# Optimization experiments

Measured on AMD Instinct MI355X. Metric: run time of the kernel, lower is better.

The kernel has to match this reference:

```python
import jax, jax.numpy as jnp
import numpy as np

B, S, D = 8, 2048, 4096   # batch, seq_len, llm_dim
H = 8                     # num_map_heads
AD = 7                    # action_dim
TD = 32                   # time_dim
HID = 256                 # hidden_dim
NBLK = 3                  # num_blocks
DH = D // H


def _layernorm(x, g, b, eps=1e-5):
    m = jnp.mean(x, axis=-1, keepdims=True)
    v = jnp.var(x, axis=-1, keepdims=True)
    return (x - m) * jax.lax.rsqrt(v + eps) * g + b


def _forward(llm_output, time, noisy_actions, probe, wq, wk, wv, bq, bk, bv,
             wo, bo, ln_g, ln_b, mlp_w1, mlp_b1, mlp_w2, mlp_b2,
             four_w, cond_w1, cond_b1, cond_w2, cond_b2,
             rin_w, rin_b, blk_ln_g, blk_ln_b, blk_w1, blk_b1, blk_w2, blk_b2,
             out_w, out_b):
    b = llm_output.shape[0]
    # --- MAPHead: learned probe attends over LLM tokens (q_len = 1) ---
    q = (jnp.broadcast_to(probe, (b, 1, D)) @ wq + bq).reshape(b, 1, H, DH)
    k = (llm_output @ wk + bk).reshape(b, S, H, DH)
    v = (llm_output @ wv + bv).reshape(b, S, H, DH)
    scores = jnp.einsum('bqhd,bkhd->bhqk', q, k) / jnp.sqrt(jnp.asarray(DH, q.dtype))
    attn = jax.nn.softmax(scores, axis=-1)
    ctx = jnp.einsum('bhqk,bkhd->bqhd', attn, v).reshape(b, 1, D)
    attn_out = ctx @ wo + bo                      # (b, 1, D)
    y = _layernorm(attn_out, ln_g, ln_b)
    h = jax.nn.gelu(y @ mlp_w1 + mlp_b1, approximate=False) @ mlp_w2 + mlp_b2
    pooled = (attn_out + h)[:, 0, :]              # (b, D)
    # --- diffusion eps-prediction network (Octo-style ScoreActor) ---
    f = 2.0 * jnp.pi * (time @ four_w.T)          # (b, TD//2) learned Fourier features
    ff = jnp.concatenate([jnp.cos(f), jnp.sin(f)], axis=-1)  # (b, TD)
    cond = jax.nn.swish(ff @ cond_w1 + cond_b1) @ cond_w2 + cond_b2
    x = jnp.concatenate([cond, pooled, noisy_actions], axis=-1)
    x = x @ rin_w + rin_b                         # (b, HID)
    for i in range(NBLK):                         # small fixed structural loop
        r = x
        x = _layernorm(x, blk_ln_g[i], blk_ln_b[i])
        x = jax.nn.swish(x @ blk_w1[i] + blk_b1[i]) @ blk_w2[i] + blk_b2[i]
        x = r + x
    x = jax.nn.swish(x)
    return x @ out_w + out_b                      # (b, AD) predicted eps


def setup_inputs() -> dict:
    key = jax.random.key(0)
    ks = iter(jax.random.split(key, 40))
    def p(shape, s=0.02):
        return jax.random.normal(next(ks), shape, dtype=jnp.float32) * s
    return {
        'llm_output': jax.random.normal(next(ks), (B, S, D), dtype=jnp.float32),
        'time': jax.random.uniform(next(ks), (B, 1), dtype=jnp.float32) * 20.0,
        'noisy_actions': jax.random.normal(next(ks), (B, AD), dtype=jnp.float32),
        'probe': p((1, 1, D)),
        'wq': p((D, D)), 'wk': p((D, D)), 'wv': p((D, D)),
        'bq': jnp.zeros((D,)), 'bk': jnp.zeros((D,)), 'bv': jnp.zeros((D,)),
        'wo': p((D, D)), 'bo': jnp.zeros((D,)),
        'ln_g': jnp.ones((D,)), 'ln_b': jnp.zeros((D,)),
        'mlp_w1': p((D, 4 * D)), 'mlp_b1': jnp.zeros((4 * D,)),
        'mlp_w2': p((4 * D, D)), 'mlp_b2': jnp.zeros((D,)),
        'four_w': p((TD // 2, 1), 1.0),
        'cond_w1': p((TD, 2 * TD)), 'cond_b1': jnp.zeros((2 * TD,)),
        'cond_w2': p((2 * TD, TD)), 'cond_b2': jnp.zeros((TD,)),
        'rin_w': p((TD + D + AD, HID)), 'rin_b': jnp.zeros((HID,)),
        'blk_ln_g': jnp.ones((NBLK, HID)), 'blk_ln_b': jnp.zeros((NBLK, HID)),
        'blk_w1': p((NBLK, HID, 4 * HID)), 'blk_b1': jnp.zeros((NBLK, 4 * HID)),
        'blk_w2': p((NBLK, 4 * HID, HID)), 'blk_b2': jnp.zeros((NBLK, HID)),
        'out_w': p((HID, AD)), 'out_b': jnp.zeros((AD,)),
    }


def reference(llm_output, time, noisy_actions, probe, wq, wk, wv, bq, bk, bv,
              wo, bo, ln_g, ln_b, mlp_w1, mlp_b1, mlp_w2, mlp_b2,
              four_w, cond_w1, cond_b1, cond_w2, cond_b2,
              rin_w, rin_b, blk_ln_g, blk_ln_b, blk_w1, blk_b1, blk_w2, blk_b2,
              out_w, out_b):
    return _forward(llm_output, time, noisy_actions, probe, wq, wk, wv, bq, bk, bv,
                    wo, bo, ln_g, ln_b, mlp_w1, mlp_b1, mlp_w2, mlp_b2,
                    four_w, cond_w1, cond_b1, cond_w2, cond_b2,
                    rin_w, rin_b, blk_ln_g, blk_ln_b, blk_w1, blk_b1, blk_w2, blk_b2,
                    out_w, out_b)
```

## Files before the change

kernel.cpp:

```cpp
#include <hip/hip_runtime.h>
#include <hip/hip_bf16.h>
#include <math.h>


#define DEV __device__ __forceinline__

DEV float warp_sum64(float v) {
    for (int o = 32; o > 0; o >>= 1) v += __shfl_down(v, o, 64);
    return v;
}

DEV float block_sum256(float v, float* sc) {
    v = warp_sum64(v);
    __syncthreads();
    if ((threadIdx.x & 63) == 0) sc[threadIdx.x >> 6] = v;
    __syncthreads();
    return sc[0] + sc[1] + sc[2] + sc[3];
}

DEV float block_max256(float v, float* sc) {
    for (int o = 32; o > 0; o >>= 1) v = fmaxf(v, __shfl_down(v, o, 64));
    __syncthreads();
    if ((threadIdx.x & 63) == 0) sc[threadIdx.x >> 6] = v;
    __syncthreads();
    return fmaxf(fmaxf(sc[0], sc[1]), fmaxf(sc[2], sc[3]));
}

DEV float swish_f(float x) { return x / (1.f + expf(-x)); }
DEV float gelu_f(float x) { return 0.5f * x * (1.f + erff(x * 0.70710678118654752f)); }

template <int NB, int VEC>
__global__ __launch_bounds__(256) void gemv_part_kernel(
    const float* __restrict__ in, const float* __restrict__ W,
    float* __restrict__ part, int I, int J, int chunk) {
    extern __shared__ float lds[];
    int tid = threadIdx.x;
    int jb = blockIdx.x, ic = blockIdx.y;
    int i0 = ic * chunk;
    int cnt = min(chunk, I - i0);
    for (int idx = tid; idx < NB * cnt; idx += 256) {
        int b = idx / cnt, ii = idx - b * cnt;
        lds[b * chunk + ii] = in[(size_t)b * I + i0 + ii];
    }
    __syncthreads();
    int j = (jb * 256 + tid) * VEC;
    float acc[NB][VEC];
#pragma unroll
    for (int b = 0; b < NB; b++)
#pragma unroll
        for (int k = 0; k < VEC; k++) acc[b][k] = 0.f;
    int ii = 0;
    for (; ii + 4 <= cnt; ii += 4) {
        float w[4][VEC];
#pragma unroll
        for (int u = 0; u < 4; u++) {
            const float* wp = W + (size_t)(i0 + ii + u) * J + j;
            if constexpr (VEC == 4) {
                float4 t = *(const float4*)wp;
                w[u][0] = t.x; w[u][1] = t.y; w[u][2] = t.z; w[u][3] = t.w;
            } else {
                w[u][0] = wp[0];
            }
        }
#pragma unroll
        for (int u = 0; u < 4; u++)
#pragma unroll
            for (int b = 0; b < NB; b++) {
                float v = lds[b * chunk + ii + u];
#pragma unroll
                for (int k = 0; k < VEC; k++) acc[b][k] = fmaf(v, w[u][k], acc[b][k]);
            }
    }
    for (; ii < cnt; ii++) {
        const float* wp = W + (size_t)(i0 + ii) * J + j;
#pragma unroll
        for (int b = 0; b < NB; b++) {
            float v = lds[b * chunk + ii];
#pragma unroll
            for (int k = 0; k < VEC; k++) acc[b][k] = fmaf(v, wp[k], acc[b][k]);
        }
    }
#pragma unroll
    for (int b = 0; b < NB; b++) {
        float* pp = part + ((size_t)ic * NB + b) * J + j;
        if constexpr (VEC == 4) {
            float4 o; o.x = acc[b][0]; o.y = acc[b][1]; o.z = acc[b][2]; o.w = acc[b][3];
            *(float4*)pp = o;
        } else {
            pp[0] = acc[b][0];
        }
    }
}

__global__ __launch_bounds__(256) void reduce_kernel(
    const float* __restrict__ part, const float* __restrict__ bias,
    const float* __restrict__ res, float* __restrict__ out,
    int NBJ, int J, int nc, int act) {
    for (int idx = blockIdx.x * 256 + threadIdx.x; idx < NBJ; idx += gridDim.x * 256) {
        float s = 0.f;
        for (int c = 0; c < nc; c++) s += part[(size_t)c * NBJ + idx];
        int j = idx % J;
        if (bias) s += bias[j];
        if (res) s += res[idx];
        if (act == 1) s = gelu_f(s);
        else if (act == 2) s = swish_f(s);
        out[idx] = s;
    }
}

__global__ __launch_bounds__(256) void qw_kernel(
    const float* __restrict__ q, const float* __restrict__ wk,
    float* __restrict__ qw) {
    int gw = blockIdx.x * 4 + (threadIdx.x >> 6);
    int lane = threadIdx.x & 63;
    int h = gw >> 12, i = gw & 4095;
    const float* wrow = wk + (size_t)i * 4096 + h * 512;
    const float* qrow = q + h * 512;
    float acc = 0.f;
#pragma unroll
    for (int k = 0; k < 8; k++) acc = fmaf(qrow[lane + 64 * k], wrow[lane + 64 * k], acc);
    acc = warp_sum64(acc);
    if (lane == 0) qw[(size_t)h * 4096 + i] = acc;
}

__global__ __launch_bounds__(256) void scores_kernel(
    const float* __restrict__ llm, const float* __restrict__ qw,
    float* __restrict__ part) {
    __shared__ float qlds[8192];
    int tid = threadIdx.x;
    int rc = blockIdx.x, cc = blockIdx.y;
    for (int idx = tid; idx < 8192; idx += 256)
        qlds[idx] = qw[(size_t)(idx >> 10) * 4096 + cc * 1024 + (idx & 1023)];
    __syncthreads();
    int wid = tid >> 6, lane = tid & 63;
    int row0 = rc * 16 + wid * 4;
    const float* base = llm + (size_t)row0 * 4096 + cc * 1024 + lane * 4;
    float acc[4][8] = {};
    for (int it = 0; it < 4; ++it) {
        float4 lv[4];
#pragma unroll
        for (int r = 0; r < 4; r++) lv[r] = *(const float4*)(base + (size_t)r * 4096 + it * 256);
#pragma unroll
        for (int h = 0; h < 8; h++) {
            float4 q4 = *(const float4*)&qlds[h * 1024 + it * 256 + lane * 4];
#pragma unroll
            for (int r = 0; r < 4; r++)
                acc[r][h] += lv[r].x * q4.x + lv[r].y * q4.y + lv[r].z * q4.z + lv[r].w * q4.w;
        }
    }
#pragma unroll
    for (int r = 0; r < 4; r++)
#pragma unroll
        for (int h = 0; h < 8; h++) acc[r][h] = warp_sum64(acc[r][h]);
    if (lane == 0) {
#pragma unroll
        for (int r = 0; r < 4; r++) {
            int row = row0 + r;
            int b = row >> 11, s = row & 2047;
#pragma unroll
            for (int h = 0; h < 8; h++)
                part[((size_t)(cc * 8 + b) * 8 + h) * 2048 + s] = acc[r][h];
        }
    }
}

__global__ __launch_bounds__(256) void softmax_kernel(
    const float* __restrict__ part, float* __restrict__ attn) {
    __shared__ float sc[4];
    int bh = blockIdx.x, tid = threadIdx.x;
    float v[8];
    float mx = -1e30f;
#pragma unroll
    for (int k = 0; k < 8; k++) {
        int s = tid + k * 256;
        float x = 0.f;
        for (int cc = 0; cc < 4; cc++) x += part[((size_t)(cc * 64 + bh)) * 2048 + s];
        x *= 0.04419417382415922f;
        v[k] = x;
        mx = fmaxf(mx, x);
    }
    float M = block_max256(mx, sc);
    float sum = 0.f;
#pragma unroll
    for (int k = 0; k < 8; k++) { v[k] = expf(v[k] - M); sum += v[k]; }
    float Sv = block_sum256(sum, sc);
    float inv = 1.f / Sv;
#pragma unroll
    for (int k = 0; k < 8; k++) attn[(size_t)bh * 2048 + tid + k * 256] = v[k] * inv;
}

__global__ __launch_bounds__(256) void pooled_kernel(
    const float* __restrict__ llm, const float* __restrict__ attn,
    float* __restrict__ part) {
    __shared__ float alds[1024];
    int tid = threadIdx.x;
    int jb = blockIdx.x, sc = blockIdx.y, b = blockIdx.z;
    for (int idx = tid; idx < 1024; idx += 256) {
        int h = idx >> 7, sl = idx & 127;
        alds[idx] = attn[((size_t)(b * 8 + h)) * 2048 + sc * 128 + sl];
    }
    __syncthreads();
    int j = jb * 1024 + tid * 4;
    const float* lbase = llm + ((size_t)(b * 2048 + sc * 128)) * 4096 + j;
    float acc[8][4] = {};
    for (int si = 0; si < 128; si += 4) {
        float4 lv[4];
#pragma unroll
        for (int u = 0; u < 4; u++) lv[u] = *(const float4*)(lbase + (size_t)(si + u) * 4096);
#pragma unroll
        for (int u = 0; u < 4; u++)
#pragma unroll
            for (int h = 0; h < 8; h++) {
                float a = alds[h * 128 + si + u];
                acc[h][0] = fmaf(a, lv[u].x, acc[h][0]);
                acc[h][1] = fmaf(a, lv[u].y, acc[h][1]);
                acc[h][2] = fmaf(a, lv[u].z, acc[h][2]);
                acc[h][3] = fmaf(a, lv[u].w, acc[h][3]);
            }
    }
#pragma unroll
    for (int h = 0; h < 8; h++) {
        float4 o; o.x = acc[h][0]; o.y = acc[h][1]; o.z = acc[h][2]; o.w = acc[h][3];
        *(float4*)(part + ((size_t)(sc * 8 + b) * 8 + h) * 4096 + j) = o;
    }
}

__global__ __launch_bounds__(256) void ctx_gemv_kernel(
    const float* __restrict__ pooled, const float* __restrict__ wv,
    float* __restrict__ part) {
    __shared__ float plds[1024];
    int tid = threadIdx.x, jb = blockIdx.x, ic = blockIdx.y;
    int i0 = ic * 64, h0 = jb * 2;
    for (int idx = tid; idx < 1024; idx += 256) {
        int b = idx >> 7, r = idx & 127, hh = r >> 6, ii = r & 63;
        plds[(b * 2 + hh) * 64 + ii] = pooled[((size_t)(b * 8 + h0 + hh)) * 4096 + i0 + ii];
    }
    __syncthreads();
    int j = jb * 1024 + tid * 4;
    int hh = tid >> 7;
    float acc[8][4] = {};
    for (int ii = 0; ii < 64; ii += 4) {
        float4 w[4];
#pragma unroll
        for (int u = 0; u < 4; u++) w[u] = *(const float4*)(wv + (size_t)(i0 + ii + u) * 4096 + j);
#pragma unroll
        for (int u = 0; u < 4; u++)
#pragma unroll
            for (int b = 0; b < 8; b++) {
                float v = plds[(b * 2 + hh) * 64 + ii + u];
                acc[b][0] = fmaf(v, w[u].x, acc[b][0]);
                acc[b][1] = fmaf(v, w[u].y, acc[b][1]);
                acc[b][2] = fmaf(v, w[u].z, acc[b][2]);
                acc[b][3] = fmaf(v, w[u].w, acc[b][3]);
            }
    }
#pragma unroll
    for (int b = 0; b < 8; b++) {
        float4 o; o.x = acc[b][0]; o.y = acc[b][1]; o.z = acc[b][2]; o.w = acc[b][3];
        *(float4*)(part + ((size_t)ic * 8 + b) * 4096 + j) = o;
    }
}

__global__ __launch_bounds__(256) void ln_kernel(
    const float* __restrict__ x, const float* __restrict__ g,
    const float* __restrict__ be, float* __restrict__ out, int N) {
    __shared__ float sc[4];
    int b = blockIdx.x, tid = threadIdx.x;
    const float* xb = x + (size_t)b * N;
    float s = 0.f, s2 = 0.f;
    for (int i = tid; i < N; i += 256) { float v = xb[i]; s += v; s2 += v * v; }
    s = block_sum256(s, sc);
    s2 = block_sum256(s2, sc);
    float mean = s / N;
    float var = s2 / N - mean * mean;
    float rstd = rsqrtf(var + 1e-5f);
    float* ob = out + (size_t)b * N;
    for (int i = tid; i < N; i += 256) {
        float v = xb[i];
        ob[i] = (v - mean) * rstd * g[i] + be[i];
    }
}

__global__ __launch_bounds__(256) void cond_kernel(
    const float* __restrict__ time, const float* __restrict__ four_w,
    const float* __restrict__ w1, const float* __restrict__ b1,
    const float* __restrict__ w2, const float* __restrict__ b2,
    float* __restrict__ cond) {
    __shared__ float ffl[256];
    __shared__ float c1[512];
    int tid = threadIdx.x;
    {
        int b = tid >> 5, jj = tid & 31;
        float f = 6.283185307179586f * time[b] * four_w[jj & 15];
        ffl[tid] = (jj < 16) ? cosf(f) : sinf(f);
    }
    __syncthreads();
    for (int idx = tid; idx < 512; idx += 256) {
        int b = idx >> 6, jj = idx & 63;
        float s = b1[jj];
        for (int i = 0; i < 32; i++) s = fmaf(ffl[b * 32 + i], w1[i * 64 + jj], s);
        c1[idx] = swish_f(s);
    }
    __syncthreads();
    {
        int b = tid >> 5, jj = tid & 31;
        float s = b2[jj];
        for (int i = 0; i < 64; i++) s = fmaf(c1[b * 64 + i], w2[i * 32 + jj], s);
        cond[b * 32 + jj] = s;
    }
}

__global__ __launch_bounds__(256) void rin_gemv_kernel(
    const float* __restrict__ cond, const float* __restrict__ pfinal,
    const float* __restrict__ noisy, const float* __restrict__ W,
    float* __restrict__ part) {
    __shared__ float lds[512];
    int tid = threadIdx.x, ic = blockIdx.x;
    int i0 = ic * 64;
    int cnt = min(64, 4135 - i0);
    for (int idx = tid; idx < 8 * cnt; idx += 256) {
        int b = idx / cnt, ii = idx - b * cnt;
        int i = i0 + ii;
        float v;
        if (i < 32) v = cond[b * 32 + i];
        else if (i < 4128) v = pfinal[(size_t)b * 4096 + i - 32];
        else v = noisy[b * 7 + i - 4128];
        lds[b * 64 + ii] = v;
    }
    __syncthreads();
    int j = tid;
    float acc[8] = {};
#pragma unroll 4
    for (int ii = 0; ii < cnt; ii++) {
        float w = W[(size_t)(i0 + ii) * 256 + j];
#pragma unroll
        for (int b = 0; b < 8; b++) acc[b] = fmaf(lds[b * 64 + ii], w, acc[b]);
    }
#pragma unroll
    for (int b = 0; b < 8; b++) part[((size_t)ic * 8 + b) * 256 + j] = acc[b];
}

__global__ __launch_bounds__(256) void final_kernel(
    const float* __restrict__ x3, const float* __restrict__ out_w,
    const float* __restrict__ out_b, float* __restrict__ out) {
    __shared__ float sw[2048];
    int tid = threadIdx.x;
    for (int idx = tid; idx < 2048; idx += 256) sw[idx] = swish_f(x3[idx]);
    __syncthreads();
    if (tid < 56) {
        int b = tid / 7, a = tid - b * 7;
        float s = out_b[a];
        for (int i = 0; i < 256; i++) s = fmaf(sw[b * 256 + i], out_w[i * 7 + a], s);
        out[tid] = s;
    }
}

extern "C" void kernel_launch(void* const* d_in, const int* in_sizes, int n_in,
                              void* d_out, int out_size, void* d_ws, size_t ws_size,
                              hipStream_t stream) {
    const float* llm     = (const float*)d_in[0];
    const float* time_   = (const float*)d_in[1];
    const float* noisy   = (const float*)d_in[2];
    const float* probe   = (const float*)d_in[3];
    const float* wq      = (const float*)d_in[4];
    const float* wk      = (const float*)d_in[5];
    const float* wv      = (const float*)d_in[6];
    const float* bq      = (const float*)d_in[7];
    const float* bv      = (const float*)d_in[9];
    const float* wo      = (const float*)d_in[10];
    const float* bo      = (const float*)d_in[11];
    const float* ln_g    = (const float*)d_in[12];
    const float* ln_b    = (const float*)d_in[13];
    const float* mlp_w1  = (const float*)d_in[14];
    const float* mlp_b1  = (const float*)d_in[15];
    const float* mlp_w2  = (const float*)d_in[16];
    const float* mlp_b2  = (const float*)d_in[17];
    const float* four_w  = (const float*)d_in[18];
    const float* cond_w1 = (const float*)d_in[19];
    const float* cond_b1 = (const float*)d_in[20];
    const float* cond_w2 = (const float*)d_in[21];
    const float* cond_b2 = (const float*)d_in[22];
    const float* rin_w   = (const float*)d_in[23];
    const float* rin_b   = (const float*)d_in[24];
    const float* bln_g   = (const float*)d_in[25];
    const float* bln_b   = (const float*)d_in[26];
    const float* bw1     = (const float*)d_in[27];
    const float* bb1     = (const float*)d_in[28];
    const float* bw2     = (const float*)d_in[29];
    const float* bb2     = (const float*)d_in[30];
    const float* out_w   = (const float*)d_in[31];
    const float* out_b   = (const float*)d_in[32];

    float* ws = (float*)d_ws;
    const size_t A = (size_t)4 * 1024 * 1024;
    float* arena    = ws;
    float* q        = ws + A;
    float* qw       = q + 4096;
    float* attn     = qw + 32768;
    float* pooled   = attn + 131072;
    float* ctx      = pooled + 262144;
    float* attn_out = ctx + 32768;
    float* y        = attn_out + 32768;
    float* h1a      = y + 32768;
    float* pfinal   = h1a + 131072;
    float* cond     = pfinal + 32768;
    float* x0       = cond + 256;
    float* xln      = x0 + 2048;
    float* g1a      = xln + 2048;
    float* x1       = g1a + 8192;
    float* x2       = x1 + 2048;
    float* x3       = x2 + 2048;

    gemv_part_kernel<1, 4><<<dim3(4, 64), 256, 1 * 64 * 4, stream>>>(probe, wq, arena, 4096, 4096, 64);
    reduce_kernel<<<16, 256, 0, stream>>>(arena, bq, nullptr, q, 4096, 4096, 64, 0);
    qw_kernel<<<8192, 256, 0, stream>>>(q, wk, qw);
    scores_kernel<<<dim3(1024, 4), 256, 0, stream>>>(llm, qw, arena);
    softmax_kernel<<<64, 256, 0, stream>>>(arena, attn);
    pooled_kernel<<<dim3(4, 16, 8), 256, 0, stream>>>(llm, attn, arena);
    reduce_kernel<<<256, 256, 0, stream>>>(arena, nullptr, nullptr, pooled, 262144, 4096, 16, 0);
    ctx_gemv_kernel<<<dim3(4, 64), 256, 0, stream>>>(pooled, wv, arena);
    reduce_kernel<<<128, 256, 0, stream>>>(arena, bv, nullptr, ctx, 32768, 4096, 64, 0);
    gemv_part_kernel<8, 4><<<dim3(4, 64), 256, 8 * 64 * 4, stream>>>(ctx, wo, arena, 4096, 4096, 64);
    reduce_kernel<<<128, 256, 0, stream>>>(arena, bo, nullptr, attn_out, 32768, 4096, 64, 0);
    ln_kernel<<<8, 256, 0, stream>>>(attn_out, ln_g, ln_b, y, 4096);
    gemv_part_kernel<8, 4><<<dim3(16, 16), 256, 8 * 256 * 4, stream>>>(y, mlp_w1, arena, 4096, 16384, 256);
    reduce_kernel<<<256, 256, 0, stream>>>(arena, mlp_b1, nullptr, h1a, 131072, 16384, 16, 1);
    gemv_part_kernel<8, 4><<<dim3(4, 64), 256, 8 * 256 * 4, stream>>>(h1a, mlp_w2, arena, 16384, 4096, 256);
    reduce_kernel<<<128, 256, 0, stream>>>(arena, mlp_b2, attn_out, pfinal, 32768, 4096, 64, 0);

    cond_kernel<<<1, 256, 0, stream>>>(time_, four_w, cond_w1, cond_b1, cond_w2, cond_b2, cond);
    rin_gemv_kernel<<<65, 256, 0, stream>>>(cond, pfinal, noisy, rin_w, arena);
    reduce_kernel<<<8, 256, 0, stream>>>(arena, rin_b, nullptr, x0, 2048, 256, 65, 0);

    float* xs[4] = {x0, x1, x2, x3};
    for (int i = 0; i < 3; i++) {
        ln_kernel<<<8, 256, 0, stream>>>(xs[i], bln_g + i * 256, bln_b + i * 256, xln, 256);
        gemv_part_kernel<8, 1><<<dim3(4, 4), 256, 8 * 64 * 4, stream>>>(
            xln, bw1 + (size_t)i * 256 * 1024, arena, 256, 1024, 64);
        reduce_kernel<<<32, 256, 0, stream>>>(arena, bb1 + i * 1024, nullptr, g1a, 8192, 1024, 4, 2);
        gemv_part_kernel<8, 1><<<dim3(1, 16), 256, 8 * 64 * 4, stream>>>(
            g1a, bw2 + (size_t)i * 1024 * 256, arena, 1024, 256, 64);
        reduce_kernel<<<8, 256, 0, stream>>>(arena, bb2 + i * 256, xs[i], xs[i + 1], 2048, 256, 16, 0);
    }
    final_kernel<<<1, 256, 0, stream>>>(x3, out_w, out_b, (float*)d_out);
}
```

Before: 1.354 ms.

## Fuse pooled reduction into ctx GEMV, fuse residual blocks, retune GEMV splits

The pooled reduce kernel is removed, and ctx_k now sums the 16 sequence-chunk partials itself while filling shared memory. Each residual block's LayerNorm, first GEMV, swish and partial reduce become one kernel (rb1_k), and its second GEMV, bias and residual add become another (rb2_k). These cut launches and intermediate global round-trips. The generic GEMV now loads 8 float4 weight rows per iteration, drops its tail handling (chunk must divide evenly), and the MLP GEMVs use 128-row chunks with more partial blocks, giving more parallelism at the cost of larger reductions.

Result: faster. 1.302 ms (-3.8%).

```diff
diff --git a/kernel.cpp b/kernel.cpp
--- a/kernel.cpp
+++ b/kernel.cpp
@@ -29,70 +29,49 @@
 DEV float swish_f(float x) { return x / (1.f + expf(-x)); }
 DEV float gelu_f(float x) { return 0.5f * x * (1.f + erff(x * 0.70710678118654752f)); }
 
-template <int NB, int VEC>
-__global__ __launch_bounds__(256) void gemv_part_kernel(
+template <int NB>
+__global__ __launch_bounds__(256) void gemvp_k(
     const float* __restrict__ in, const float* __restrict__ W,
     float* __restrict__ part, int I, int J, int chunk) {
     extern __shared__ float lds[];
     int tid = threadIdx.x;
     int jb = blockIdx.x, ic = blockIdx.y;
     int i0 = ic * chunk;
-    int cnt = min(chunk, I - i0);
-    for (int idx = tid; idx < NB * cnt; idx += 256) {
-        int b = idx / cnt, ii = idx - b * cnt;
-        lds[b * chunk + ii] = in[(size_t)b * I + i0 + ii];
-    }
-    __syncthreads();
-    int j = (jb * 256 + tid) * VEC;
-    float acc[NB][VEC];
+    for (int idx = tid; idx < NB * chunk; idx += 256) {
+        int b = idx / chunk, ii = idx - b * chunk;
+        lds[idx] = in[(size_t)b * I + i0 + ii];
+    }
+    __syncthreads();
+    int j = (jb * 256 + tid) * 4;
+    float acc[NB][4];
 #pragma unroll
     for (int b = 0; b < NB; b++)
 #pragma unroll
-        for (int k = 0; k < VEC; k++) acc[b][k] = 0.f;
-    int ii = 0;
-    for (; ii + 4 <= cnt; ii += 4) {
-        float w[4][VEC];
-#pragma unroll
-        for (int u = 0; u < 4; u++) {
-            const float* wp = W + (size_t)(i0 + ii + u) * J + j;
-            if constexpr (VEC == 4) {
-                float4 t = *(const float4*)wp;
-                w[u][0] = t.x; w[u][1] = t.y; w[u][2] = t.z; w[u][3] = t.w;
-            } else {
-                w[u][0] = wp[0];
-            }
-        }
-#pragma unroll
-        for (int u = 0; u < 4; u++)
+        for (int k = 0; k < 4; k++) acc[b][k] = 0.f;
+    const float* wbase = W + (size_t)i0 * J + j;
+    for (int ii = 0; ii < chunk; ii += 8) {
+        float4 w[8];
+#pragma unroll
+        for (int u = 0; u < 8; u++) w[u] = *(const float4*)(wbase + (size_t)(ii + u) * J);
+#pragma unroll
+        for (int u = 0; u < 8; u++)
 #pragma unroll
             for (int b = 0; b < NB; b++) {
                 float v = lds[b * chunk + ii + u];
-#pragma unroll
-                for (int k = 0; k < VEC; k++) acc[b][k] = fmaf(v, w[u][k], acc[b][k]);
+                acc[b][0] = fmaf(v, w[u].x, acc[b][0]);
+                acc[b][1] = fmaf(v, w[u].y, acc[b][1]);
+                acc[b][2] = fmaf(v, w[u].z, acc[b][2]);
+                acc[b][3] = fmaf(v, w[u].w, acc[b][3]);
             }
     }
-    for (; ii < cnt; ii++) {
-        const float* wp = W + (size_t)(i0 + ii) * J + j;
-#pragma unroll
-        for (int b = 0; b < NB; b++) {
-            float v = lds[b * chunk + ii];
-#pragma unroll
-            for (int k = 0; k < VEC; k++) acc[b][k] = fmaf(v, wp[k], acc[b][k]);
-        }
-    }
 #pragma unroll
     for (int b = 0; b < NB; b++) {
-        float* pp = part + ((size_t)ic * NB + b) * J + j;
-        if constexpr (VEC == 4) {
-            float4 o; o.x = acc[b][0]; o.y = acc[b][1]; o.z = acc[b][2]; o.w = acc[b][3];
-            *(float4*)pp = o;
-        } else {
-            pp[0] = acc[b][0];
-        }
-    }
-}
-
-__global__ __launch_bounds__(256) void reduce_kernel(
+        float4 o; o.x = acc[b][0]; o.y = acc[b][1]; o.z = acc[b][2]; o.w = acc[b][3];
+        *(float4*)(part + ((size_t)ic * NB + b) * J + j) = o;
+    }
+}
+
+__global__ __launch_bounds__(256) void reduce_k(
     const float* __restrict__ part, const float* __restrict__ bias,
     const float* __restrict__ res, float* __restrict__ out,
     int NBJ, int J, int nc, int act) {
@@ -108,7 +87,7 @@
     }
 }
 
-__global__ __launch_bounds__(256) void qw_kernel(
+__global__ __launch_bounds__(256) void qw_k(
     const float* __restrict__ q, const float* __restrict__ wk,
     float* __restrict__ qw) {
     int gw = blockIdx.x * 4 + (threadIdx.x >> 6);
@@ -123,7 +102,7 @@
     if (lane == 0) qw[(size_t)h * 4096 + i] = acc;
 }
 
-__global__ __launch_bounds__(256) void scores_kernel(
+__global__ __launch_bounds__(256) void scores_k(
     const float* __restrict__ llm, const float* __restrict__ qw,
     float* __restrict__ part) {
     __shared__ float qlds[8192];
@@ -164,7 +143,7 @@
     }
 }
 
-__global__ __launch_bounds__(256) void softmax_kernel(
+__global__ __launch_bounds__(256) void softmax_k(
     const float* __restrict__ part, float* __restrict__ attn) {
     __shared__ float sc[4];
     int bh = blockIdx.x, tid = threadIdx.x;
@@ -189,7 +168,7 @@
     for (int k = 0; k < 8; k++) attn[(size_t)bh * 2048 + tid + k * 256] = v[k] * inv;
 }
 
-__global__ __launch_bounds__(256) void pooled_kernel(
+__global__ __launch_bounds__(256) void pooled_k(
     const float* __restrict__ llm, const float* __restrict__ attn,
     float* __restrict__ part) {
     __shared__ float alds[1024];
@@ -203,12 +182,12 @@
     int j = jb * 1024 + tid * 4;
     const float* lbase = llm + ((size_t)(b * 2048 + sc * 128)) * 4096 + j;
     float acc[8][4] = {};
-    for (int si = 0; si < 128; si += 4) {
-        float4 lv[4];
-#pragma unroll
-        for (int u = 0; u < 4; u++) lv[u] = *(const float4*)(lbase + (size_t)(si + u) * 4096);
-#pragma unroll
-        for (int u = 0; u < 4; u++)
+    for (int si = 0; si < 128; si += 8) {
+        float4 lv[8];
+#pragma unroll
+        for (int u = 0; u < 8; u++) lv[u] = *(const float4*)(lbase + (size_t)(si + u) * 4096);
+#pragma unroll
+        for (int u = 0; u < 8; u++)
 #pragma unroll
             for (int h = 0; h < 8; h++) {
                 float a = alds[h * 128 + si + u];
@@ -225,26 +204,30 @@
     }
 }
 
-__global__ __launch_bounds__(256) void ctx_gemv_kernel(
-    const float* __restrict__ pooled, const float* __restrict__ wv,
+__global__ __launch_bounds__(256) void ctx_k(
+    const float* __restrict__ ppart, const float* __restrict__ wv,
     float* __restrict__ part) {
     __shared__ float plds[1024];
     int tid = threadIdx.x, jb = blockIdx.x, ic = blockIdx.y;
     int i0 = ic * 64, h0 = jb * 2;
     for (int idx = tid; idx < 1024; idx += 256) {
         int b = idx >> 7, r = idx & 127, hh = r >> 6, ii = r & 63;
-        plds[(b * 2 + hh) * 64 + ii] = pooled[((size_t)(b * 8 + h0 + hh)) * 4096 + i0 + ii];
+        float s = 0.f;
+#pragma unroll 4
+        for (int sc = 0; sc < 16; sc++)
+            s += ppart[((size_t)(sc * 8 + b) * 8 + h0 + hh) * 4096 + i0 + ii];
+        plds[(b * 2 + hh) * 64 + ii] = s;
     }
     __syncthreads();
     int j = jb * 1024 + tid * 4;
     int hh = tid >> 7;
     float acc[8][4] = {};
-    for (int ii = 0; ii < 64; ii += 4) {
-        float4 w[4];
-#pragma unroll
-        for (int u = 0; u < 4; u++) w[u] = *(const float4*)(wv + (size_t)(i0 + ii + u) * 4096 + j);
-#pragma unroll
-        for (int u = 0; u < 4; u++)
+    for (int ii = 0; ii < 64; ii += 8) {
+        float4 w[8];
+#pragma unroll
+        for (int u = 0; u < 8; u++) w[u] = *(const float4*)(wv + (size_t)(i0 + ii + u) * 4096 + j);
+#pragma unroll
+        for (int u = 0; u < 8; u++)
 #pragma unroll
             for (int b = 0; b < 8; b++) {
                 float v = plds[(b * 2 + hh) * 64 + ii + u];
@@ -261,7 +244,7 @@
     }
 }
 
-__global__ __launch_bounds__(256) void ln_kernel(
+__global__ __launch_bounds__(256) void ln_k(
     const float* __restrict__ x, const float* __restrict__ g,
     const float* __restrict__ be, float* __restrict__ out, int N) {
     __shared__ float sc[4];
@@ -281,7 +264,7 @@
     }
 }
 
-__global__ __launch_bounds__(256) void cond_kernel(
+__global__ __launch_bounds__(256) void cond_k(
     const float* __restrict__ time, const float* __restrict__ four_w,
     const float* __restrict__ w1, const float* __restrict__ b1,
     const float* __restrict__ w2, const float* __restrict__ b2,
@@ -310,7 +293,7 @@
     }
 }
 
-__global__ __launch_bounds__(256) void rin_gemv_kernel(
+__global__ __launch_bounds__(256) void rin_k(
     const float* __restrict__ cond, const float* __restrict__ pfinal,
     const float* __restrict__ noisy, const float* __restrict__ W,
     float* __restrict__ part) {
@@ -340,7 +323,95 @@
     for (int b = 0; b < 8; b++) part[((size_t)ic * 8 + b) * 256 + j] = acc[b];
 }
 
-__global__ __launch_bounds__(256) void final_kernel(
+__global__ __launch_bounds__(256) void rb1_k(
+    const float* __restrict__ xin, const float* __restrict__ g,
+    const float* __restrict__ be, const float* __restrict__ W1,
+    const float* __restrict__ b1, float* __restrict__ g1) {
+    __shared__ float xn[2048];
+    __shared__ float red[2048];
+    __shared__ float sm[8], sv[8];
+    int tid = threadIdx.x, jb = blockIdx.x;
+    int b = tid >> 5, l = tid & 31;
+    float xv[8];
+    float s = 0.f, s2 = 0.f;
+#pragma unroll
+    for (int k = 0; k < 8; k++) {
+        float v = xin[tid * 8 + k];
+        xv[k] = v; s += v; s2 += v * v;
+    }
+    for (int o = 16; o > 0; o >>= 1) { s += __shfl_down(s, o, 32); s2 += __shfl_down(s2, o, 32); }
+    if (l == 0) { sm[b] = s; sv[b] = s2; }
+    __syncthreads();
+    float mean = sm[b] / 256.f;
+    float rstd = rsqrtf(sv[b] / 256.f - mean * mean + 1e-5f);
+#pragma unroll
+    for (int k = 0; k < 8; k++) {
+        int i = (tid * 8 + k) & 255;
+        xn[tid * 8 + k] = (xv[k] - mean) * rstd * g[i] + be[i];
+    }
+    __syncthreads();
+    int jj = tid & 63, ig = tid >> 6;
+    int j = jb * 64 + jj;
+    float acc[8] = {};
+    for (int i = ig * 64; i < ig * 64 + 64; i += 4) {
+        float w[4];
+#pragma unroll
+        for (int u = 0; u < 4; u++) w[u] = W1[(size_t)(i + u) * 1024 + j];
+#pragma unroll
+        for (int u = 0; u < 4; u++)
+#pragma unroll
+            for (int bb = 0; bb < 8; bb++) acc[bb] = fmaf(xn[bb * 256 + i + u], w[u], acc[bb]);
+    }
+#pragma unroll
+    for (int bb = 0; bb < 8; bb++) red[tid * 8 + bb] = acc[bb];
+    __syncthreads();
+#pragma unroll
+    for (int t = 0; t < 2; t++) {
+        int idx = tid * 2 + t;
+        int ojj = idx >> 3, ob = idx & 7;
+        float v = red[ojj * 8 + ob] + red[512 + ojj * 8 + ob] +
+                  red[1024 + ojj * 8 + ob] + red[1536 + ojj * 8 + ob];
+        v += b1[jb * 64 + ojj];
+        g1[(size_t)ob * 1024 + jb * 64 + ojj] = swish_f(v);
+    }
+}
+
+__global__ __launch_bounds__(256) void rb2_k(
+    const float* __restrict__ g1, const float* __restrict__ W2,
+    const float* __restrict__ b2, const float* __restrict__ xres,
+    float* __restrict__ xout) {
+    __shared__ float gl[8192];
+    __shared__ float red[2048];
+    int tid = threadIdx.x, jb = blockIdx.x;
+    for (int idx = tid * 4; idx < 8192; idx += 1024)
+        *(float4*)&gl[idx] = *(const float4*)&g1[idx];
+    __syncthreads();
+    int jj = tid & 15, ig = tid >> 4;
+    int j = jb * 16 + jj;
+    float acc[8] = {};
+    for (int i = ig * 64; i < ig * 64 + 64; i += 4) {
+        float w[4];
+#pragma unroll
+        for (int u = 0; u < 4; u++) w[u] = W2[(size_t)(i + u) * 256 + j];
+#pragma unroll
+        for (int u = 0; u < 4; u++)
+#pragma unroll
+            for (int bb = 0; bb < 8; bb++) acc[bb] = fmaf(gl[bb * 1024 + i + u], w[u], acc[bb]);
+    }
+#pragma unroll
+    for (int bb = 0; bb < 8; bb++) red[tid * 8 + bb] = acc[bb];
+    __syncthreads();
+    if (tid < 128) {
+        int ojj = tid >> 3, ob = tid & 7;
+        float v = 0.f;
+#pragma unroll
+        for (int ig2 = 0; ig2 < 16; ig2++) v += red[(ig2 * 16 + ojj) * 8 + ob];
+        int oj = jb * 16 + ojj;
+        xout[(size_t)ob * 256 + oj] = v + b2[oj] + xres[(size_t)ob * 256 + oj];
+    }
+}
+
+__global__ __launch_bounds__(256) void final_k(
     const float* __restrict__ x3, const float* __restrict__ out_w,
     const float* __restrict__ out_b, float* __restrict__ out) {
     __shared__ float sw[2048];
@@ -394,53 +465,48 @@
     float* ws = (float*)d_ws;
     const size_t A = (size_t)4 * 1024 * 1024;
     float* arena    = ws;
-    float* q        = ws + A;
+    float* arena2   = ws + A;
+    float* q        = arena2 + 2097152;
     float* qw       = q + 4096;
     float* attn     = qw + 32768;
-    float* pooled   = attn + 131072;
-    float* ctx      = pooled + 262144;
+    float* ctx      = attn + 131072;
     float* attn_out = ctx + 32768;
     float* y        = attn_out + 32768;
     float* h1a      = y + 32768;
     float* pfinal   = h1a + 131072;
     float* cond     = pfinal + 32768;
     float* x0       = cond + 256;
-    float* xln      = x0 + 2048;
-    float* g1a      = xln + 2048;
+    float* g1a      = x0 + 2048;
     float* x1       = g1a + 8192;
     float* x2       = x1 + 2048;
     float* x3       = x2 + 2048;
 
-    gemv_part_kernel<1, 4><<<dim3(4, 64), 256, 1 * 64 * 4, stream>>>(probe, wq, arena, 4096, 4096, 64);
-    reduce_kernel<<<16, 256, 0, stream>>>(arena, bq, nullptr, q, 4096, 4096, 64, 0);
-    qw_kernel<<<8192, 256, 0, stream>>>(q, wk, qw);
-    scores_kernel<<<dim3(1024, 4), 256, 0, stream>>>(llm, qw, arena);
-    softmax_kernel<<<64, 256, 0, stream>>>(arena, attn);
-    pooled_kernel<<<dim3(4, 16, 8), 256, 0, stream>>>(llm, attn, arena);
-    reduce_kernel<<<256, 256, 0, stream>>>(arena, nullptr, nullptr, pooled, 262144, 4096, 16, 0);
-    ctx_gemv_kernel<<<dim3(4, 64), 256, 0, stream>>>(pooled, wv, arena);
-    reduce_kernel<<<128, 256, 0, stream>>>(arena, bv, nullptr, ctx, 32768, 4096, 64, 0);
-    gemv_part_kernel<8, 4><<<dim3(4, 64), 256, 8 * 64 * 4, stream>>>(ctx, wo, arena, 4096, 4096, 64);
-    reduce_kernel<<<128, 256, 0, stream>>>(arena, bo, nullptr, attn_out, 32768, 4096, 64, 0);
-    ln_kernel<<<8, 256, 0, stream>>>(attn_out, ln_g, ln_b, y, 4096);
-    gemv_part_kernel<8, 4><<<dim3(16, 16), 256, 8 * 256 * 4, stream>>>(y, mlp_w1, arena, 4096, 16384, 256);
-    reduce_kernel<<<256, 256, 0, stream>>>(arena, mlp_b1, nullptr, h1a, 131072, 16384, 16, 1);
-    gemv_part_kernel<8, 4><<<dim3(4, 64), 256, 8 * 256 * 4, stream>>>(h1a, mlp_w2, arena, 16384, 4096, 256);
-    reduce_kernel<<<128, 256, 0, stream>>>(arena, mlp_b2, attn_out, pfinal, 32768, 4096, 64, 0);
-
-    cond_kernel<<<1, 256, 0, stream>>>(time_, four_w, cond_w1, cond_b1, cond_w2, cond_b2, cond);
-    rin_gemv_kernel<<<65, 256, 0, stream>>>(cond, pfinal, noisy, rin_w, arena);
-    reduce_kernel<<<8, 256, 0, stream>>>(arena, rin_b, nullptr, x0, 2048, 256, 65, 0);
+    gemvp_k<1><<<dim3(4, 64), 256, 64 * 4, stream>>>(probe, wq, arena, 4096, 4096, 64);
+    reduce_k<<<16, 256, 0, stream>>>(arena, bq, nullptr, q, 4096, 4096, 64, 0);
+    qw_k<<<8192, 256, 0, stream>>>(q, wk, qw);
+    scores_k<<<dim3(1024, 4), 256, 0, stream>>>(llm, qw, arena);
+    softmax_k<<<64, 256, 0, stream>>>(arena, attn);
+    pooled_k<<<dim3(4, 16, 8), 256, 0, stream>>>(llm, attn, arena);
+    ctx_k<<<dim3(4, 64), 256, 0, stream>>>(arena, wv, arena2);
+    reduce_k<<<32, 256, 0, stream>>>(arena2, bv, nullptr, ctx, 32768, 4096, 64, 0);
+    gemvp_k<8><<<dim3(4, 64), 256, 8 * 64 * 4, stream>>>(ctx, wo, arena, 4096, 4096, 64);
+    reduce_k<<<32, 256, 0, stream>>>(arena, bo, nullptr, attn_out, 32768, 4096, 64, 0);
+    ln_k<<<8, 256, 0, stream>>>(attn_out, ln_g, ln_b, y, 4096);
+    gemvp_k<8><<<dim3(16, 32), 256, 8 * 128 * 4, stream>>>(y, mlp_w1, arena, 4096, 16384, 128);
+    reduce_k<<<256, 256, 0, stream>>>(arena, mlp_b1, nullptr, h1a, 131072, 16384, 32, 1);
+    gemvp_k<8><<<dim3(4, 128), 256, 8 * 128 * 4, stream>>>(h1a, mlp_w2, arena, 16384, 4096, 128);
+    reduce_k<<<64, 256, 0, stream>>>(arena, mlp_b2, attn_out, pfinal, 32768, 4096, 128, 0);
+
+    cond_k<<<1, 256, 0, stream>>>(time_, four_w, cond_w1, cond_b1, cond_w2, cond_b2, cond);
+    rin_k<<<65, 256, 0, stream>>>(cond, pfinal, noisy, rin_w, arena);
+    reduce_k<<<8, 256, 0, stream>>>(arena, rin_b, nullptr, x0, 2048, 256, 65, 0);
 
     float* xs[4] = {x0, x1, x2, x3};
     for (int i = 0; i < 3; i++) {
-        ln_kernel<<<8, 256, 0, stream>>>(xs[i], bln_g + i * 256, bln_b + i * 256, xln, 256);
-        gemv_part_kernel<8, 1><<<dim3(4, 4), 256, 8 * 64 * 4, stream>>>(
-            xln, bw1 + (size_t)i * 256 * 1024, arena, 256, 1024, 64);
-        reduce_kernel<<<32, 256, 0, stream>>>(arena, bb1 + i * 1024, nullptr, g1a, 8192, 1024, 4, 2);
-        gemv_part_kernel<8, 1><<<dim3(1, 16), 256, 8 * 64 * 4, stream>>>(
-            g1a, bw2 + (size_t)i * 1024 * 256, arena, 1024, 256, 64);
-        reduce_kernel<<<8, 256, 0, stream>>>(arena, bb2 + i * 256, xs[i], xs[i + 1], 2048, 256, 16, 0);
-    }
-    final_kernel<<<1, 256, 0, stream>>>(x3, out_w, out_b, (float*)d_out);
-}
+        rb1_k<<<16, 256, 0, stream>>>(xs[i], bln_g + i * 256, bln_b + i * 256,
+                                      bw1 + (size_t)i * 256 * 1024, bb1 + i * 1024, g1a);
+        rb2_k<<<16, 256, 0, stream>>>(g1a, bw2 + (size_t)i * 1024 * 256, bb2 + i * 256,
+                                      xs[i], xs[i + 1]);
+    }
+    final_k<<<1, 256, 0, stream>>>(x3, out_w, out_b, (float*)d_out);
+}
```
